# Performance work log

Hardware: AMD Instinct MI355X
Metric: run time of the kernel (lower is better)

Reference implementation:

```python
import jax, jax.numpy as jnp
import numpy as np
import math

EMBED_DIM = 768
NUM_HEADS = 12
HEAD_DIM = EMBED_DIM // NUM_HEADS
B, L = 8, 1024


def setup_inputs() -> dict:
    key = jax.random.key(0)
    ks = jax.random.split(key, 10)
    s = 1.0 / math.sqrt(EMBED_DIM)
    x = jax.random.normal(ks[0], (B, L, EMBED_DIM), dtype=jnp.float32)
    attention_mask = jnp.ones((B, L), dtype=jnp.int32)
    # torch nn.Linear weights: shape (out, in), y = x @ W.T + b
    Wq = jax.random.normal(ks[1], (EMBED_DIM, EMBED_DIM), jnp.float32) * s
    bq = jnp.zeros((EMBED_DIM,), jnp.float32)
    Wk = jax.random.normal(ks[2], (EMBED_DIM, EMBED_DIM), jnp.float32) * s
    bk = jnp.zeros((EMBED_DIM,), jnp.float32)
    Wv = jax.random.normal(ks[3], (EMBED_DIM, EMBED_DIM), jnp.float32) * s
    bv = jnp.zeros((EMBED_DIM,), jnp.float32)
    Wo = jax.random.normal(ks[4], (EMBED_DIM, EMBED_DIM), jnp.float32) * s
    bo = jnp.zeros((EMBED_DIM,), jnp.float32)
    return {"x": x, "attention_mask": attention_mask,
            "Wq": Wq, "bq": bq, "Wk": Wk, "bk": bk,
            "Wv": Wv, "bv": bv, "Wo": Wo, "bo": bo}


def reference(x, attention_mask, Wq, bq, Wk, bk, Wv, bv, Wo, bo):
    # NOTE: faithful to the original buggy forward:
    #   V = K_embed(x); scores = K @ K^T; Q unused; scale by sqrt(embed_dim);
    #   mask broadcasts over the KEY axis (masks entire query rows).
    b, l, d = x.shape
    K = x @ Wk.T + bk                                  # (B,L,D)
    Q = x @ Wq.T + bq                                  # computed but unused (as in source)
    V = K                                              # V = self.K_embed(x)
    Kh = K.reshape(b, l, NUM_HEADS, HEAD_DIM).transpose(0, 2, 1, 3)  # (B,H,L,dh)
    Vh = V.reshape(b, l, NUM_HEADS, HEAD_DIM).transpose(0, 2, 1, 3)
    scores = jnp.einsum('bhid,bhjd->bhij', Kh, Kh) / math.sqrt(EMBED_DIM)
    if attention_mask is not None:
        row_mask = attention_mask[:, None, :, None]    # (B,1,L,1) -> masks query rows
        scores = jnp.where(row_mask == 0, jnp.float32(-1e9), scores)
    attn = jax.nn.softmax(scores, axis=-1)             # dropout p=0 -> identity
    wV = jnp.einsum('bhij,bhjd->bhid', attn, Vh)       # (B,H,L,dh)
    wV = wV.transpose(0, 2, 1, 3).reshape(b, l, d)     # (B,L,D)
    out = wV @ Wo.T + bo
    return out
```

## Files before the change

### kernel.cpp

```cpp
#include <hip/hip_runtime.h>
#include <hip/hip_bf16.h>

#define NUM_B 8
#define SEQ 1024
#define DIM 768
#define NH 12
#define DH 64

typedef __attribute__((ext_vector_type(8))) short bf16x8;
typedef __attribute__((ext_vector_type(4))) float floatx4;
typedef __attribute__((ext_vector_type(4))) unsigned short ushortx4;
typedef __attribute__((ext_vector_type(8))) unsigned short ushortx8;

__device__ __forceinline__ unsigned short f2bf(float f) {
  unsigned u = __float_as_uint(f);
  u += 0x7FFFu + ((u >> 16) & 1u);
  return (unsigned short)(u >> 16);
}

#define GLOAD16(g, l) __builtin_amdgcn_global_load_lds( \
    (const __attribute__((address_space(1))) unsigned int*)(g), \
    (__attribute__((address_space(3))) unsigned int*)(l), 16, 0, 0)

__global__ __launch_bounds__(256) void convert_kernel(
    const float* __restrict__ x, const float* __restrict__ Wk,
    const float* __restrict__ Wo, unsigned short* __restrict__ xb,
    unsigned short* __restrict__ Wkb, unsigned short* __restrict__ Wob)
{
  const int NX4 = (8192 * 768) / 4;
  const int NW4 = (768 * 768) / 4;
  int i = blockIdx.x * 256 + threadIdx.x;
  const float* s; unsigned short* d; int off;
  if (i < NX4)            { s = x;  d = xb;  off = i; }
  else if (i < NX4 + NW4) { s = Wk; d = Wkb; off = i - NX4; }
  else                    { s = Wo; d = Wob; off = i - NX4 - NW4; }
  float4 v = ((const float4*)s)[off];
  ushortx4 h;
  h.x = f2bf(v.x); h.y = f2bf(v.y); h.z = f2bf(v.z); h.w = f2bf(v.w);
  ((ushortx4*)d)[off] = h;
}

__global__ __launch_bounds__(256) void proj_k_kernel(
    const unsigned short* __restrict__ xb, const unsigned short* __restrict__ Wkb,
    const float* __restrict__ bk, unsigned short* __restrict__ Kbh,
    unsigned short* __restrict__ KbhT)
{
  __shared__ __align__(16) unsigned short smem[24576];
  const int tid = threadIdx.x;
  const int lane = tid & 63;
  const int w = tid >> 6;
  const int wr = w >> 1, wc = w & 1;
  const int quad = lane >> 4, r16 = lane & 15;
  const int rs = r16 & 7;
  const int m0 = blockIdx.x * 64, n0 = blockIdx.y * 128;
  const int wbase = (tid & ~63);

  floatx4 acc[2][4] = {};

  auto stage = [&](int kt, int buf) {
    unsigned short* As = smem + buf * 12288;
    unsigned short* Bs = As + 4096;
#pragma unroll
    for (int i = 0; i < 2; ++i) {
      int c = tid + i * 256;
      int row = c >> 3, g = (c & 7) ^ (row & 7);
      GLOAD16(xb + (size_t)(m0 + row) * DIM + kt + g * 8,
              As + (size_t)(wbase + i * 256) * 8);
    }
#pragma unroll
    for (int i = 0; i < 4; ++i) {
      int c = tid + i * 256;
      int row = c >> 3, g = (c & 7) ^ (row & 7);
      GLOAD16(Wkb + (size_t)(n0 + row) * DIM + kt + g * 8,
              Bs + (size_t)(wbase + i * 256) * 8);
    }
  };

  stage(0, 0);
  int buf = 0;
  for (int it = 0; it < 12; ++it) {
    __syncthreads();
    if (it + 1 < 12) stage((it + 1) * 64, buf ^ 1);
    const unsigned short* As = smem + buf * 12288;
    const unsigned short* Bs = As + 4096;
    bf16x8 af[2][2], bfm[4][2];
#pragma unroll
    for (int mi = 0; mi < 2; ++mi)
#pragma unroll
      for (int kc = 0; kc < 2; ++kc)
        af[mi][kc] = *(const bf16x8*)&As[(wr * 32 + mi * 16 + r16) * 64 + ((kc * 4 + quad) ^ rs) * 8];
#pragma unroll
    for (int ni = 0; ni < 4; ++ni)
#pragma unroll
      for (int kc = 0; kc < 2; ++kc)
        bfm[ni][kc] = *(const bf16x8*)&Bs[(wc * 64 + ni * 16 + r16) * 64 + ((kc * 4 + quad) ^ rs) * 8];
#pragma unroll
    for (int mi = 0; mi < 2; ++mi)
#pragma unroll
      for (int ni = 0; ni < 4; ++ni) {
        acc[mi][ni] = __builtin_amdgcn_mfma_f32_16x16x32_bf16(af[mi][0], bfm[ni][0], acc[mi][ni], 0, 0, 0);
        acc[mi][ni] = __builtin_amdgcn_mfma_f32_16x16x32_bf16(af[mi][1], bfm[ni][1], acc[mi][ni], 0, 0, 0);
      }
    buf ^= 1;
  }

  __syncthreads();
  unsigned short* Ct = smem;
  const int bb = m0 >> 10, l0 = m0 & 1023;
#pragma unroll
  for (int mi = 0; mi < 2; ++mi)
#pragma unroll
    for (int ni = 0; ni < 4; ++ni) {
      int col = n0 + wc * 64 + ni * 16 + r16;
      float bias = bk[col];
      int hh = col >> 6, dd = col & 63;
      ushortx4 pk;
#pragma unroll
      for (int r = 0; r < 4; ++r) {
        int mrow = wr * 32 + mi * 16 + quad * 4 + r;
        unsigned short us = f2bf(acc[mi][ni][r] + bias);
        Kbh[((size_t)(bb * NH + hh) * SEQ + l0 + mrow) * DH + dd] = us;
        pk[r] = us;
      }
      *(ushortx4*)&Ct[(wc * 64 + ni * 16 + r16) * 72 + wr * 32 + mi * 16 + quad * 4] = pk;
    }
  __syncthreads();
#pragma unroll
  for (int i = 0; i < 4; ++i) {
    int c = tid + i * 256;
    int row = c >> 3, ch = c & 7;
    ushortx8 v = *(const ushortx8*)&Ct[row * 72 + ch * 8];
    int j = n0 + row;
    int hh = j >> 6, dd = j & 63;
    *(ushortx8*)&KbhT[((size_t)(bb * NH + hh) * DH + dd) * SEQ + l0 + ch * 8] = v;
  }
}

__global__ __launch_bounds__(256) void attn_kernel(
    const unsigned short* __restrict__ Kbh, const unsigned short* __restrict__ KbhT,
    const int* __restrict__ mask, unsigned short* __restrict__ wV)
{
  __shared__ __align__(16) unsigned short smem[25344];
  unsigned short* Ps = smem + 16384;
  float* rsum = (float*)&smem[25088];

  const int tid = threadIdx.x;
  const int lane = tid & 63;
  const int w = tid >> 6;
  const int quad = lane >> 4, r16 = lane & 15;
  const int rs = r16 & 7;
  const int qt = blockIdx.x, bh = blockIdx.y;
  const int b = bh / NH, h = bh % NH;
  const unsigned short* Kb  = Kbh  + (size_t)bh * SEQ * DH;
  const unsigned short* KbT = KbhT + (size_t)bh * DH * SEQ;
  const int q0 = qt * 128;
  const int qw = w * 32;
  const int wbase = (tid & ~63);
  const float SCALE = 0.036084391824351615f;

  bf16x8 aq[2][2];
#pragma unroll
  for (int nt = 0; nt < 2; ++nt)
#pragma unroll
    for (int kc = 0; kc < 2; ++kc)
      aq[nt][kc] = *(const bf16x8*)(Kb + (size_t)(q0 + qw + nt * 16 + r16) * DH + kc * 32 + quad * 8);

  float scm[2];
#pragma unroll
  for (int nt = 0; nt < 2; ++nt)
    scm[nt] = (mask[b * SEQ + q0 + qw + nt * 16 + r16] != 0) ? SCALE : 0.0f;

  floatx4 accO[2][4] = {};
  float psum[2] = {};

  auto stage = [&](int kt, int buf) {
    unsigned short* Ks  = smem + buf * 4096;
    unsigned short* KTs = smem + 8192 + buf * 4096;
#pragma unroll
    for (int i = 0; i < 2; ++i) {
      int c = tid + i * 256;
      int row = c >> 3, g = (c & 7) ^ (row & 7);
      GLOAD16(Kb + (size_t)(kt + row) * DH + g * 8,
              Ks + (size_t)(wbase + i * 256) * 8);
    }
#pragma unroll
    for (int i = 0; i < 2; ++i) {
      int c = tid + i * 256;
      int row = c >> 3, g = (c & 7) ^ (row & 7);
      GLOAD16(KbT + (size_t)row * SEQ + kt + g * 8,
              KTs + (size_t)(wbase + i * 256) * 8);
    }
  };

  stage(0, 0);
  int buf = 0;
  for (int it = 0; it < SEQ / 64; ++it) {
    __syncthreads();
    if (it + 1 < SEQ / 64) stage((it + 1) * 64, buf ^ 1);
    const unsigned short* Ks  = smem + buf * 4096;
    const unsigned short* KTs = smem + 8192 + buf * 4096;

    floatx4 St[4][2] = {};
#pragma unroll
    for (int kt = 0; kt < 4; ++kt) {
      int rb = (kt * 16 + r16) * 64;
      bf16x8 k0 = *(const bf16x8*)&Ks[rb + ((quad) ^ rs) * 8];
      bf16x8 k1 = *(const bf16x8*)&Ks[rb + ((4 + quad) ^ rs) * 8];
#pragma unroll
      for (int nt = 0; nt < 2; ++nt) {
        St[kt][nt] = __builtin_amdgcn_mfma_f32_16x16x32_bf16(k0, aq[nt][0], St[kt][nt], 0, 0, 0);
        St[kt][nt] = __builtin_amdgcn_mfma_f32_16x16x32_bf16(k1, aq[nt][1], St[kt][nt], 0, 0, 0);
      }
    }

#pragma unroll
    for (int nt = 0; nt < 2; ++nt) {
      float sc = scm[nt];
      int prow = (qw + nt * 16 + r16) * 68 + quad * 4;
#pragma unroll
      for (int kt = 0; kt < 4; ++kt) {
        float p0 = __expf(St[kt][nt][0] * sc);
        float p1 = __expf(St[kt][nt][1] * sc);
        float p2 = __expf(St[kt][nt][2] * sc);
        float p3 = __expf(St[kt][nt][3] * sc);
        psum[nt] += (p0 + p1) + (p2 + p3);
        __hip_bfloat162 lo = __float22bfloat162_rn(make_float2(p0, p1));
        __hip_bfloat162 hi = __float22bfloat162_rn(make_float2(p2, p3));
        unsigned u0, u1;
        __builtin_memcpy(&u0, &lo, 4);
        __builtin_memcpy(&u1, &hi, 4);
        *(uint2*)&Ps[prow + kt * 16] = make_uint2(u0, u1);
      }
    }

    bf16x8 ap[2][2];
#pragma unroll
    for (int mi = 0; mi < 2; ++mi)
#pragma unroll
      for (int kc = 0; kc < 2; ++kc)
        ap[mi][kc] = *(const bf16x8*)&Ps[(qw + mi * 16 + r16) * 68 + kc * 32 + quad * 8];
#pragma unroll
    for (int ni = 0; ni < 4; ++ni) {
      int rb = (ni * 16 + r16) * 64;
      bf16x8 v0 = *(const bf16x8*)&KTs[rb + ((quad) ^ rs) * 8];
      bf16x8 v1 = *(const bf16x8*)&KTs[rb + ((4 + quad) ^ rs) * 8];
#pragma unroll
      for (int mi = 0; mi < 2; ++mi) {
        accO[mi][ni] = __builtin_amdgcn_mfma_f32_16x16x32_bf16(ap[mi][0], v0, accO[mi][ni], 0, 0, 0);
        accO[mi][ni] = __builtin_amdgcn_mfma_f32_16x16x32_bf16(ap[mi][1], v1, accO[mi][ni], 0, 0, 0);
      }
    }
    buf ^= 1;
  }

#pragma unroll
  for (int nt = 0; nt < 2; ++nt) {
    float s = psum[nt];
    s += __shfl_xor(s, 16);
    s += __shfl_xor(s, 32);
    psum[nt] = s;
  }
  if (quad == 0) {
#pragma unroll
    for (int nt = 0; nt < 2; ++nt)
      rsum[qw + nt * 16 + r16] = psum[nt];
  }
  float rinv[2][4];
#pragma unroll
  for (int mi = 0; mi < 2; ++mi)
#pragma unroll
    for (int r = 0; r < 4; ++r)
      rinv[mi][r] = 1.0f / rsum[qw + mi * 16 + quad * 4 + r];

#pragma unroll
  for (int mi = 0; mi < 2; ++mi)
#pragma unroll
    for (int ni = 0; ni < 4; ++ni)
#pragma unroll
      for (int r = 0; r < 4; ++r) {
        int l = q0 + qw + mi * 16 + quad * 4 + r;
        int col = h * DH + ni * 16 + r16;
        wV[(size_t)(b * SEQ + l) * DIM + col] = f2bf(accO[mi][ni][r] * rinv[mi][r]);
      }
}

__global__ __launch_bounds__(256) void proj_o_kernel(
    const unsigned short* __restrict__ wVb, const unsigned short* __restrict__ Wob,
    const float* __restrict__ bo, float* __restrict__ out)
{
  __shared__ __align__(16) unsigned short smem[24576];
  const int tid = threadIdx.x;
  const int lane = tid & 63;
  const int w = tid >> 6;
  const int wr = w >> 1, wc = w & 1;
  const int quad = lane >> 4, r16 = lane & 15;
  const int rs = r16 & 7;
  const int m0 = blockIdx.x * 64, n0 = blockIdx.y * 128;
  const int wbase = (tid & ~63);

  floatx4 acc[2][4] = {};

  auto stage = [&](int kt, int buf) {
    unsigned short* As = smem + buf * 12288;
    unsigned short* Bs = As + 4096;
#pragma unroll
    for (int i = 0; i < 2; ++i) {
      int c = tid + i * 256;
      int row = c >> 3, g = (c & 7) ^ (row & 7);
      GLOAD16(wVb + (size_t)(m0 + row) * DIM + kt + g * 8,
              As + (size_t)(wbase + i * 256) * 8);
    }
#pragma unroll
    for (int i = 0; i < 4; ++i) {
      int c = tid + i * 256;
      int row = c >> 3, g = (c & 7) ^ (row & 7);
      GLOAD16(Wob + (size_t)(n0 + row) * DIM + kt + g * 8,
              Bs + (size_t)(wbase + i * 256) * 8);
    }
  };

  stage(0, 0);
  int buf = 0;
  for (int it = 0; it < 12; ++it) {
    __syncthreads();
    if (it + 1 < 12) stage((it + 1) * 64, buf ^ 1);
    const unsigned short* As = smem + buf * 12288;
    const unsigned short* Bs = As + 4096;
    bf16x8 af[2][2], bfm[4][2];
#pragma unroll
    for (int mi = 0; mi < 2; ++mi)
#pragma unroll
      for (int kc = 0; kc < 2; ++kc)
        af[mi][kc] = *(const bf16x8*)&As[(wr * 32 + mi * 16 + r16) * 64 + ((kc * 4 + quad) ^ rs) * 8];
#pragma unroll
    for (int ni = 0; ni < 4; ++ni)
#pragma unroll
      for (int kc = 0; kc < 2; ++kc)
        bfm[ni][kc] = *(const bf16x8*)&Bs[(wc * 64 + ni * 16 + r16) * 64 + ((kc * 4 + quad) ^ rs) * 8];
#pragma unroll
    for (int mi = 0; mi < 2; ++mi)
#pragma unroll
      for (int ni = 0; ni < 4; ++ni) {
        acc[mi][ni] = __builtin_amdgcn_mfma_f32_16x16x32_bf16(af[mi][0], bfm[ni][0], acc[mi][ni], 0, 0, 0);
        acc[mi][ni] = __builtin_amdgcn_mfma_f32_16x16x32_bf16(af[mi][1], bfm[ni][1], acc[mi][ni], 0, 0, 0);
      }
    buf ^= 1;
  }

#pragma unroll
  for (int mi = 0; mi < 2; ++mi)
#pragma unroll
    for (int ni = 0; ni < 4; ++ni) {
      int col = n0 + wc * 64 + ni * 16 + r16;
      float bias = bo[col];
#pragma unroll
      for (int r = 0; r < 4; ++r) {
        int row = m0 + wr * 32 + mi * 16 + quad * 4 + r;
        out[(size_t)row * DIM + col] = acc[mi][ni][r] + bias;
      }
    }
}

extern "C" void kernel_launch(void* const* d_in, const int* in_sizes, int n_in,
                              void* d_out, int out_size, void* d_ws, size_t ws_size,
                              hipStream_t stream) {
  const float* x  = (const float*)d_in[0];
  const int* mask = (const int*)d_in[1];
  const float* Wk = (const float*)d_in[4];
  const float* bk = (const float*)d_in[5];
  const float* Wo = (const float*)d_in[8];
  const float* bo = (const float*)d_in[9];
  float* out = (float*)d_out;

  unsigned short* p = (unsigned short*)d_ws;
  unsigned short* xb   = p;  p += (size_t)8192 * 768;
  unsigned short* Wkb  = p;  p += (size_t)768 * 768;
  unsigned short* Wob  = p;  p += (size_t)768 * 768;
  unsigned short* Kbh  = p;  p += (size_t)NUM_B * NH * SEQ * DH;
  unsigned short* KbhT = p;  p += (size_t)NUM_B * NH * SEQ * DH;
  unsigned short* wVb  = p;

  convert_kernel<<<7296, 256, 0, stream>>>(x, Wk, Wo, xb, Wkb, Wob);
  proj_k_kernel<<<dim3(128, 6), 256, 0, stream>>>(xb, Wkb, bk, Kbh, KbhT);
  attn_kernel<<<dim3(8, NUM_B * NH), 256, 0, stream>>>(Kbh, KbhT, mask, wVb);
  proj_o_kernel<<<dim3(128, 6), 256, 0, stream>>>(wVb, Wob, bo, out);
}
```

Baseline: 181.7 us.

## Keep softmax probabilities in registers for PV MFMA and drop LDS swizzle

The attention kernel no longer writes the probability tile to shared memory and reads it back. The exponentiated scores are kept in registers and fed straight into 16x16x16 bf16 MFMAs, whose operand layout matches the score accumulator layout, and the V operand is read from LDS as 4-element chunks. Separately, the XOR swizzle on all shared-memory tiles (both projection GEMMs and attention) is replaced by plain row-major indexing. Dropping the swizzle may bring back LDS bank conflicts on the 16-byte reads with a 64-element row stride. The smaller MFMA shape doubles the instruction count for the PV product.

```diff
diff --git a/kernel.cpp b/kernel.cpp
--- a/kernel.cpp
+++ b/kernel.cpp
@@ -8,6 +8,7 @@
 #define DH 64
 
 typedef __attribute__((ext_vector_type(8))) short bf16x8;
+typedef __attribute__((ext_vector_type(4))) short bf16x4;
 typedef __attribute__((ext_vector_type(4))) float floatx4;
 typedef __attribute__((ext_vector_type(4))) unsigned short ushortx4;
 typedef __attribute__((ext_vector_type(8))) unsigned short ushortx8;
@@ -16,6 +17,15 @@
   unsigned u = __float_as_uint(f);
   u += 0x7FFFu + ((u >> 16) & 1u);
   return (unsigned short)(u >> 16);
+}
+
+__device__ __forceinline__ floatx4 mfma16(bf16x4 a, bf16x4 b, floatx4 c) {
+#if __has_builtin(__builtin_amdgcn_mfma_f32_16x16x16bf16_1k)
+  return __builtin_amdgcn_mfma_f32_16x16x16bf16_1k(a, b, c, 0, 0, 0);
+#else
+  asm("v_mfma_f32_16x16x16_bf16 %0, %1, %2, %3" : "=v"(c) : "v"(a), "v"(b), "v"(c));
+  return c;
+#endif
 }
 
 #define GLOAD16(g, l) __builtin_amdgcn_global_load_lds( \
@@ -51,7 +61,6 @@
   const int w = tid >> 6;
   const int wr = w >> 1, wc = w & 1;
   const int quad = lane >> 4, r16 = lane & 15;
-  const int rs = r16 & 7;
   const int m0 = blockIdx.x * 64, n0 = blockIdx.y * 128;
   const int wbase = (tid & ~63);
 
@@ -63,14 +72,14 @@
 #pragma unroll
     for (int i = 0; i < 2; ++i) {
       int c = tid + i * 256;
-      int row = c >> 3, g = (c & 7) ^ (row & 7);
+      int row = c >> 3, g = c & 7;
       GLOAD16(xb + (size_t)(m0 + row) * DIM + kt + g * 8,
               As + (size_t)(wbase + i * 256) * 8);
     }
 #pragma unroll
     for (int i = 0; i < 4; ++i) {
       int c = tid + i * 256;
-      int row = c >> 3, g = (c & 7) ^ (row & 7);
+      int row = c >> 3, g = c & 7;
       GLOAD16(Wkb + (size_t)(n0 + row) * DIM + kt + g * 8,
               Bs + (size_t)(wbase + i * 256) * 8);
     }
@@ -88,12 +97,12 @@
     for (int mi = 0; mi < 2; ++mi)
 #pragma unroll
       for (int kc = 0; kc < 2; ++kc)
-        af[mi][kc] = *(const bf16x8*)&As[(wr * 32 + mi * 16 + r16) * 64 + ((kc * 4 + quad) ^ rs) * 8];
+        af[mi][kc] = *(const bf16x8*)&As[(wr * 32 + mi * 16 + r16) * 64 + kc * 32 + quad * 8];
 #pragma unroll
     for (int ni = 0; ni < 4; ++ni)
 #pragma unroll
       for (int kc = 0; kc < 2; ++kc)
-        bfm[ni][kc] = *(const bf16x8*)&Bs[(wc * 64 + ni * 16 + r16) * 64 + ((kc * 4 + quad) ^ rs) * 8];
+        bfm[ni][kc] = *(const bf16x8*)&Bs[(wc * 64 + ni * 16 + r16) * 64 + kc * 32 + quad * 8];
 #pragma unroll
     for (int mi = 0; mi < 2; ++mi)
 #pragma unroll
@@ -140,15 +149,13 @@
     const unsigned short* __restrict__ Kbh, const unsigned short* __restrict__ KbhT,
     const int* __restrict__ mask, unsigned short* __restrict__ wV)
 {
-  __shared__ __align__(16) unsigned short smem[25344];
-  unsigned short* Ps = smem + 16384;
-  float* rsum = (float*)&smem[25088];
+  __shared__ __align__(16) unsigned short smem[16640];
+  float* rsum = (float*)&smem[16384];
 
   const int tid = threadIdx.x;
   const int lane = tid & 63;
   const int w = tid >> 6;
   const int quad = lane >> 4, r16 = lane & 15;
-  const int rs = r16 & 7;
   const int qt = blockIdx.x, bh = blockIdx.y;
   const int b = bh / NH, h = bh % NH;
   const unsigned short* Kb  = Kbh  + (size_t)bh * SEQ * DH;
@@ -179,14 +186,13 @@
 #pragma unroll
     for (int i = 0; i < 2; ++i) {
       int c = tid + i * 256;
-      int row = c >> 3, g = (c & 7) ^ (row & 7);
-      GLOAD16(Kb + (size_t)(kt + row) * DH + g * 8,
+      GLOAD16(Kb + (size_t)kt * DH + (size_t)c * 8,
               Ks + (size_t)(wbase + i * 256) * 8);
     }
 #pragma unroll
     for (int i = 0; i < 2; ++i) {
       int c = tid + i * 256;
-      int row = c >> 3, g = (c & 7) ^ (row & 7);
+      int row = c >> 3, g = c & 7;
       GLOAD16(KbT + (size_t)row * SEQ + kt + g * 8,
               KTs + (size_t)(wbase + i * 256) * 8);
     }
@@ -204,8 +210,8 @@
 #pragma unroll
     for (int kt = 0; kt < 4; ++kt) {
       int rb = (kt * 16 + r16) * 64;
-      bf16x8 k0 = *(const bf16x8*)&Ks[rb + ((quad) ^ rs) * 8];
-      bf16x8 k1 = *(const bf16x8*)&Ks[rb + ((4 + quad) ^ rs) * 8];
+      bf16x8 k0 = *(const bf16x8*)&Ks[rb + quad * 8];
+      bf16x8 k1 = *(const bf16x8*)&Ks[rb + 32 + quad * 8];
 #pragma unroll
       for (int nt = 0; nt < 2; ++nt) {
         St[kt][nt] = __builtin_amdgcn_mfma_f32_16x16x32_bf16(k0, aq[nt][0], St[kt][nt], 0, 0, 0);
@@ -213,10 +219,10 @@
       }
     }
 
+    bf16x4 pf[4][2];
 #pragma unroll
     for (int nt = 0; nt < 2; ++nt) {
       float sc = scm[nt];
-      int prow = (qw + nt * 16 + r16) * 68 + quad * 4;
 #pragma unroll
       for (int kt = 0; kt < 4; ++kt) {
         float p0 = __expf(St[kt][nt][0] * sc);
@@ -229,25 +235,20 @@
         unsigned u0, u1;
         __builtin_memcpy(&u0, &lo, 4);
         __builtin_memcpy(&u1, &hi, 4);
-        *(uint2*)&Ps[prow + kt * 16] = make_uint2(u0, u1);
-      }
-    }
-
-    bf16x8 ap[2][2];
-#pragma unroll
-    for (int mi = 0; mi < 2; ++mi)
-#pragma unroll
-      for (int kc = 0; kc < 2; ++kc)
-        ap[mi][kc] = *(const bf16x8*)&Ps[(qw + mi * 16 + r16) * 68 + kc * 32 + quad * 8];
+        uint2 t = make_uint2(u0, u1);
+        __builtin_memcpy(&pf[kt][nt], &t, 8);
+      }
+    }
+
 #pragma unroll
     for (int ni = 0; ni < 4; ++ni) {
       int rb = (ni * 16 + r16) * 64;
-      bf16x8 v0 = *(const bf16x8*)&KTs[rb + ((quad) ^ rs) * 8];
-      bf16x8 v1 = *(const bf16x8*)&KTs[rb + ((4 + quad) ^ rs) * 8];
-#pragma unroll
-      for (int mi = 0; mi < 2; ++mi) {
-        accO[mi][ni] = __builtin_amdgcn_mfma_f32_16x16x32_bf16(ap[mi][0], v0, accO[mi][ni], 0, 0, 0);
-        accO[mi][ni] = __builtin_amdgcn_mfma_f32_16x16x32_bf16(ap[mi][1], v1, accO[mi][ni], 0, 0, 0);
+#pragma unroll
+      for (int kt = 0; kt < 4; ++kt) {
+        bf16x4 bv = *(const bf16x4*)&KTs[rb + kt * 16 + quad * 4];
+#pragma unroll
+        for (int mi = 0; mi < 2; ++mi)
+          accO[mi][ni] = mfma16(pf[kt][mi], bv, accO[mi][ni]);
       }
     }
     buf ^= 1;
@@ -294,7 +295,6 @@
   const int w = tid >> 6;
   const int wr = w >> 1, wc = w & 1;
   const int quad = lane >> 4, r16 = lane & 15;
-  const int rs = r16 & 7;
   const int m0 = blockIdx.x * 64, n0 = blockIdx.y * 128;
   const int wbase = (tid & ~63);
 
@@ -306,14 +306,14 @@
 #pragma unroll
     for (int i = 0; i < 2; ++i) {
       int c = tid + i * 256;
-      int row = c >> 3, g = (c & 7) ^ (row & 7);
+      int row = c >> 3, g = c & 7;
       GLOAD16(wVb + (size_t)(m0 + row) * DIM + kt + g * 8,
               As + (size_t)(wbase + i * 256) * 8);
     }
 #pragma unroll
     for (int i = 0; i < 4; ++i) {
       int c = tid + i * 256;
-      int row = c >> 3, g = (c & 7) ^ (row & 7);
+      int row = c >> 3, g = c & 7;
       GLOAD16(Wob + (size_t)(n0 + row) * DIM + kt + g * 8,
               Bs + (size_t)(wbase + i * 256) * 8);
     }
@@ -331,12 +331,12 @@
     for (int mi = 0; mi < 2; ++mi)
 #pragma unroll
       for (int kc = 0; kc < 2; ++kc)
-        af[mi][kc] = *(const bf16x8*)&As[(wr * 32 + mi * 16 + r16) * 64 + ((kc * 4 + quad) ^ rs) * 8];
+        af[mi][kc] = *(const bf16x8*)&As[(wr * 32 + mi * 16 + r16) * 64 + kc * 32 + quad * 8];
 #pragma unroll
     for (int ni = 0; ni < 4; ++ni)
 #pragma unroll
       for (int kc = 0; kc < 2; ++kc)
-        bfm[ni][kc] = *(const bf16x8*)&Bs[(wc * 64 + ni * 16 + r16) * 64 + ((kc * 4 + quad) ^ rs) * 8];
+        bfm[ni][kc] = *(const bf16x8*)&Bs[(wc * 64 + ni * 16 + r16) * 64 + kc * 32 + quad * 8];
 #pragma unroll
     for (int mi = 0; mi < 2; ++mi)
 #pragma unroll
```

Measured after the change: 235.4 us. 29.5% more time.
